# Optimization experiments

Measured on AMD Instinct MI355X. Metric: run time of the kernel, lower is better.

The kernel has to match this reference:

```python
import jax, jax.numpy as jnp
import numpy as np

B, C, D, H, W = 2, 128, 16, 16, 16

def setup_inputs() -> dict:
    key = jax.random.key(0)
    ks = jax.random.split(key, 7)
    s = 0.02
    return {
        "x": jax.random.normal(ks[0], (B, C, D, H, W), jnp.float32),
        "Wq": jax.random.normal(ks[1], (C, C), jnp.float32) * s,
        "bq": jax.random.normal(ks[2], (C,), jnp.float32) * s,
        "Wk": jax.random.normal(ks[3], (C, C), jnp.float32) * s,
        "bk": jax.random.normal(ks[4], (C,), jnp.float32) * s,
        "Wv": jax.random.normal(ks[5], (C, C), jnp.float32) * s,
        "bv": jax.random.normal(ks[6], (C,), jnp.float32) * s,
    }

def reference(x, Wq, bq, Wk, bk, Wv, bv):
    b, c, d, h, w = x.shape
    n = d * h * w
    xf = x.reshape(b, c, n)  # [B, C, N]
    # 1x1x1 Conv3d == per-voxel linear over channels
    q = jnp.einsum('oc,bcn->bon', Wq, xf) + bq[None, :, None]
    k = jnp.einsum('oc,bcn->bon', Wk, xf) + bk[None, :, None]
    v = jnp.einsum('oc,bcn->bon', Wv, xf) + bv[None, :, None]
    # energy[b,n,m] = sum_c q[b,c,n] * k[b,c,m]  (no scale, as in source)
    energy = jnp.einsum('bcn,bcm->bnm', q, k)
    attention = jax.nn.softmax(energy, axis=-1)
    # out[b,c,n] = sum_m v[b,c,m] * attention[b,n,m]
    out = jnp.einsum('bcm,bnm->bcn', v, attention)
    return out.reshape(b, c, d, h, w)
```

## Files before the change

### kernel.cpp

```cpp
#include <hip/hip_runtime.h>


typedef __bf16 bf16x8 __attribute__((ext_vector_type(8)));
typedef __bf16 bf16x4v __attribute__((ext_vector_type(4)));
typedef float  f32x4  __attribute__((ext_vector_type(4)));

#define LDP 136
#define LDO 33
#define QB_STRIDE 132
#define VB_STRIDE 36

constexpr int CB = 128;
constexpr int NB = 4096;
constexpr int BB = 2;

__device__ __forceinline__ bf16x8 ldfrag(const __bf16* lds, int row, int koff, int ld) {
  return *(const bf16x8*)(lds + row * ld + koff);
}

__device__ __forceinline__ unsigned cvt_pk_bf16(float lo, float hi) {
  unsigned w;
  asm("v_cvt_pk_bf16_f32 %0, %1, %2" : "=v"(w) : "v"(lo), "v"(hi));
  return w;
}

__global__ __launch_bounds__(256) void qkv_fused_kernel(
    const float* __restrict__ x,
    const float* __restrict__ Wq, const float* __restrict__ bq,
    const float* __restrict__ Wk, const float* __restrict__ bk,
    const float* __restrict__ Wv, const float* __restrict__ bv,
    __bf16* __restrict__ Qt, __bf16* __restrict__ Kt, __bf16* __restrict__ Vo)
{
  extern __shared__ __align__(16) char smem_raw[];
  __bf16* xT = (__bf16*)smem_raw;
  __bf16* Wl = xT + 32 * LDP;
  float* bounce = (float*)(Wl + 128 * LDP);

  const int b  = blockIdx.y;
  const int n0 = blockIdx.x * 32;
  const int t  = threadIdx.x;
  const int lane = t & 63, w = t >> 6;
  const int l15 = lane & 15, quad = lane >> 4;
  const int nstrip = (w & 1) * 16;
  const int obase  = (w >> 1) * 64;

#pragma unroll
  for (int u = 0; u < 4; u++) {
    int v = t + u * 256;
    int c = v >> 3, i4 = v & 7;
    float4 d = *(const float4*)(x + (size_t)(b * CB + c) * NB + n0 + i4 * 4);
    xT[(i4 * 4 + 0) * LDP + c] = (__bf16)d.x;
    xT[(i4 * 4 + 1) * LDP + c] = (__bf16)d.y;
    xT[(i4 * 4 + 2) * LDP + c] = (__bf16)d.z;
    xT[(i4 * 4 + 3) * LDP + c] = (__bf16)d.w;
  }

  auto store_m = [&](int mm) {
    if (mm < 2) {
      const float* bp = (mm == 0) ? bq : bk;
      const float qs = (mm == 0) ? 1.4426950408889634f : 1.0f;
      __bf16* O = (mm == 0) ? Qt : Kt;
#pragma unroll
      for (int u = 0; u < 2; u++) {
        int v = t + u * 256;
        int n = v >> 4, c8 = (v & 15) * 8;
        f32x4 p0 = *(const f32x4*)(bounce + n * QB_STRIDE + c8);
        f32x4 p1 = *(const f32x4*)(bounce + n * QB_STRIDE + c8 + 4);
        float4 b0 = *(const float4*)(bp + c8);
        float4 b1 = *(const float4*)(bp + c8 + 4);
        bf16x8 o8;
        o8[0] = (__bf16)((p0[0] + b0.x) * qs);
        o8[1] = (__bf16)((p0[1] + b0.y) * qs);
        o8[2] = (__bf16)((p0[2] + b0.z) * qs);
        o8[3] = (__bf16)((p0[3] + b0.w) * qs);
        o8[4] = (__bf16)((p1[0] + b1.x) * qs);
        o8[5] = (__bf16)((p1[1] + b1.y) * qs);
        o8[6] = (__bf16)((p1[2] + b1.z) * qs);
        o8[7] = (__bf16)((p1[3] + b1.w) * qs);
        *(bf16x8*)(O + (size_t)(b * NB + n0 + n) * CB + c8) = o8;
      }
    } else {
#pragma unroll
      for (int u = 0; u < 2; u++) {
        int v = t + u * 256;
        int o = v >> 2, n8 = (v & 3) * 8;
        float bias = bv[o];
        f32x4 p0 = *(const f32x4*)(bounce + o * VB_STRIDE + n8);
        f32x4 p1 = *(const f32x4*)(bounce + o * VB_STRIDE + n8 + 4);
        bf16x8 o8;
        o8[0] = (__bf16)(p0[0] + bias);
        o8[1] = (__bf16)(p0[1] + bias);
        o8[2] = (__bf16)(p0[2] + bias);
        o8[3] = (__bf16)(p0[3] + bias);
        o8[4] = (__bf16)(p1[0] + bias);
        o8[5] = (__bf16)(p1[1] + bias);
        o8[6] = (__bf16)(p1[2] + bias);
        o8[7] = (__bf16)(p1[3] + bias);
        *(bf16x8*)(Vo + (size_t)(b * CB + o) * NB + n0 + n8) = o8;
      }
    }
  };

#pragma unroll
  for (int m = 0; m < 3; m++) {
    const float* W = (m == 0) ? Wq : (m == 1) ? Wk : Wv;
#pragma unroll
    for (int u = 0; u < 16; u++) {
      int v = t + u * 256;
      int o = v >> 5, c4 = v & 31;
      float4 d = *(const float4*)(W + o * 128 + c4 * 4);
      bf16x4v uu = {(__bf16)d.x, (__bf16)d.y, (__bf16)d.z, (__bf16)d.w};
      *(bf16x4v*)(Wl + o * LDP + c4 * 4) = uu;
    }
    if (m > 0) store_m(m - 1);
    __syncthreads();

    if (m < 2) {
      f32x4 acc[4] = {(f32x4)0.0f, (f32x4)0.0f, (f32x4)0.0f, (f32x4)0.0f};
#pragma unroll
      for (int ks = 0; ks < 4; ks++) {
        int koff = ks * 32 + quad * 8;
        bf16x8 a = ldfrag(xT, nstrip + l15, koff, LDP);
#pragma unroll
        for (int ct = 0; ct < 4; ct++) {
          bf16x8 bb = ldfrag(Wl, obase + ct * 16 + l15, koff, LDP);
          acc[ct] = __builtin_amdgcn_mfma_f32_16x16x32_bf16(a, bb, acc[ct], 0, 0, 0);
        }
      }
#pragma unroll
      for (int ct = 0; ct < 4; ct++)
#pragma unroll
        for (int r = 0; r < 4; r++)
          bounce[(nstrip + quad * 4 + r) * QB_STRIDE + obase + ct * 16 + l15] =
              acc[ct][r];
    } else {
      f32x4 acc[4] = {(f32x4)0.0f, (f32x4)0.0f, (f32x4)0.0f, (f32x4)0.0f};
#pragma unroll
      for (int ks = 0; ks < 4; ks++) {
        int koff = ks * 32 + quad * 8;
        bf16x8 bb = ldfrag(xT, nstrip + l15, koff, LDP);
#pragma unroll
        for (int rr = 0; rr < 4; rr++) {
          bf16x8 a = ldfrag(Wl, obase + rr * 16 + l15, koff, LDP);
          acc[rr] = __builtin_amdgcn_mfma_f32_16x16x32_bf16(a, bb, acc[rr], 0, 0, 0);
        }
      }
#pragma unroll
      for (int rr = 0; rr < 4; rr++)
#pragma unroll
        for (int r = 0; r < 4; r++)
          bounce[(obase + rr * 16 + quad * 4 + r) * VB_STRIDE + nstrip + l15] =
              acc[rr][r];
    }
    __syncthreads();
  }
  store_m(2);
}

__global__ __launch_bounds__(256, 2) void attn_part_kernel(
    const __bf16* __restrict__ Qt,
    const __bf16* __restrict__ Kt,
    const __bf16* __restrict__ Vo,
    __bf16* __restrict__ Opart, float* __restrict__ Ll, int ksz)
{
  extern __shared__ __align__(16) char smem_raw[];

  const int b  = blockIdx.y;
  const int q0 = blockIdx.x * 128;
  const int s  = blockIdx.z;
  const int k_base = s * ksz;
  const int nit = ksz >> 6;
  const int t  = threadIdx.x;
  const int lane = t & 63, w = t >> 6;
  const int l15 = lane & 15, quad = lane >> 4;
  const int row0 = w * 32;
  const int xsw = (l15 & 7) << 4;

  bf16x8 qf[2][4];
#pragma unroll
  for (int qt = 0; qt < 2; qt++)
#pragma unroll
    for (int cb = 0; cb < 4; cb++)
      qf[qt][cb] = *(const bf16x8*)(Qt +
          (size_t)(b * NB + q0 + row0 + qt * 16 + l15) * CB + cb * 32 + quad * 8);

  bf16x8 kr[4], vr[4];
  auto load_tile = [&](int m0) {
#pragma unroll
    for (int u = 0; u < 4; u++) {
      int v = t + u * 256;
      int j = v >> 4, c8 = v & 15;
      kr[u] = *(const bf16x8*)(Kt + (size_t)(b * NB + m0 + j) * CB + c8 * 8);
    }
#pragma unroll
    for (int u = 0; u < 4; u++) {
      int v = t + u * 256;
      int c = v >> 3, j8 = v & 7;
      vr[u] = *(const bf16x8*)(Vo + (size_t)(b * CB + c) * NB + m0 + j8 * 8);
    }
  };
  auto write_tile = [&](int bf) {
    char* Kn = smem_raw + bf * 32768;
    char* Vn = Kn + 16384;
#pragma unroll
    for (int u = 0; u < 4; u++) {
      int v = t + u * 256;
      int j = v >> 4, c8 = v & 15;
      *(bf16x8*)(Kn + j * 256 + ((c8 * 16) ^ ((j & 7) << 4))) = kr[u];
    }
#pragma unroll
    for (int u = 0; u < 4; u++) {
      int v = t + u * 256;
      int c = v >> 3, j8 = v & 7;
      *(bf16x8*)(Vn + c * 128 + ((j8 * 16) ^ ((c & 7) << 4))) = vr[u];
    }
  };

  float lsum[2] = {0.0f, 0.0f};
  f32x4 o_acc[2][8];
#pragma unroll
  for (int qt = 0; qt < 2; qt++)
#pragma unroll
    for (int tt = 0; tt < 8; tt++) o_acc[qt][tt] = (f32x4)0.0f;

  load_tile(k_base);
  write_tile(0);
  __syncthreads();

  int cur = 0;
  for (int it = 0; it < nit; it++) {
    if (it + 1 < nit) load_tile(k_base + (it + 1) * 64);

    const char* Kc = smem_raw + cur * 32768;
    const char* Vc = Kc + 16384;

    f32x4 sacc[2][4];
#pragma unroll
    for (int qt = 0; qt < 2; qt++)
#pragma unroll
      for (int kt = 0; kt < 4; kt++) sacc[qt][kt] = (f32x4)0.0f;
#pragma unroll
    for (int cb = 0; cb < 4; cb++) {
      const int xo = (cb * 64 + quad * 16) ^ xsw;
#pragma unroll
      for (int kt = 0; kt < 4; kt++) {
        bf16x8 af = *(const bf16x8*)(Kc + (kt * 16 + l15) * 256 + xo);
        sacc[0][kt] = __builtin_amdgcn_mfma_f32_16x16x32_bf16(af, qf[0][cb], sacc[0][kt], 0, 0, 0);
        sacc[1][kt] = __builtin_amdgcn_mfma_f32_16x16x32_bf16(af, qf[1][cb], sacc[1][kt], 0, 0, 0);
      }
    }

    bf16x8 pa[2][2];
#pragma unroll
    for (int qt = 0; qt < 2; qt++) {
      unsigned d[4][2];
#pragma unroll
      for (int kt = 0; kt < 4; kt++) {
        float p0 = exp2f(sacc[qt][kt][0]);
        float p1 = exp2f(sacc[qt][kt][1]);
        float p2 = exp2f(sacc[qt][kt][2]);
        float p3 = exp2f(sacc[qt][kt][3]);
        lsum[qt] += (p0 + p1) + (p2 + p3);
        d[kt][0] = cvt_pk_bf16(p0, p1);
        d[kt][1] = cvt_pk_bf16(p2, p3);
      }
#pragma unroll
      for (int ks = 0; ks < 2; ks++) {
        unsigned a0 = d[2 * ks][0], a1 = d[2 * ks][1];
        unsigned b0 = d[2 * ks + 1][0], b1 = d[2 * ks + 1][1];
        asm("v_permlane32_swap_b32 %0, %1" : "+v"(a0), "+v"(b0));
        asm("v_permlane16_swap_b32 %0, %1" : "+v"(a0), "+v"(b0));
        asm("v_permlane32_swap_b32 %0, %1" : "+v"(a1), "+v"(b1));
        asm("v_permlane16_swap_b32 %0, %1" : "+v"(a1), "+v"(b1));
        union { unsigned u[4]; bf16x8 v; } pk;
        pk.u[0] = a0; pk.u[1] = a1; pk.u[2] = b0; pk.u[3] = b1;
        pa[qt][ks] = pk.v;
      }
    }

#pragma unroll
    for (int ks = 0; ks < 2; ks++) {
      const int xo = (ks * 64 + quad * 16) ^ xsw;
#pragma unroll
      for (int tt = 0; tt < 8; tt++) {
        bf16x8 bb = *(const bf16x8*)(Vc + (tt * 16 + l15) * 128 + xo);
        o_acc[0][tt] = __builtin_amdgcn_mfma_f32_16x16x32_bf16(pa[0][ks], bb, o_acc[0][tt], 0, 0, 0);
        o_acc[1][tt] = __builtin_amdgcn_mfma_f32_16x16x32_bf16(pa[1][ks], bb, o_acc[1][tt], 0, 0, 0);
      }
    }

    if (it + 1 < nit) {
      write_tile(cur ^ 1);
      __syncthreads();
      cur ^= 1;
    }
  }

#pragma unroll
  for (int qt = 0; qt < 2; qt++) {
    lsum[qt] += __shfl_xor(lsum[qt], 16);
    lsum[qt] += __shfl_xor(lsum[qt], 32);
  }

  const size_t obase = ((size_t)(s * BB + b) * NB + q0) * CB;
#pragma unroll
  for (int qt = 0; qt < 2; qt++)
#pragma unroll
    for (int tt = 0; tt < 8; tt++)
#pragma unroll
      for (int r = 0; r < 4; r++)
        Opart[obase + (size_t)(row0 + qt * 16 + quad * 4 + r) * CB + tt * 16 + l15] =
            (__bf16)o_acc[qt][tt][r];
  if (quad == 0) {
    const size_t lbase = (size_t)(s * BB + b) * NB + q0 + row0;
#pragma unroll
    for (int qt = 0; qt < 2; qt++)
      Ll[lbase + qt * 16 + l15] = lsum[qt];
  }
}

__global__ __launch_bounds__(256) void combine_kernel(
    const __bf16* __restrict__ Opart, const float* __restrict__ Ll,
    float* __restrict__ out, int nsplit)
{
  extern __shared__ __align__(16) char smem_raw[];
  float* Olf = (float*)smem_raw;

  const int b  = blockIdx.y;
  const int n0 = blockIdx.x * 64;
  const int c0 = blockIdx.z * 32;
  const int t  = threadIdx.x;
  const int i  = t >> 2;
  const int cc = (t & 3) * 8;

  float L = 0.0f;
  for (int s = 0; s < nsplit; s++)
    L += Ll[(size_t)(s * BB + b) * NB + n0 + i];

  float acc[8];
#pragma unroll
  for (int u = 0; u < 8; u++) acc[u] = 0.0f;
  for (int s = 0; s < nsplit; s++) {
    bf16x8 d = *(const bf16x8*)(Opart +
        ((size_t)(s * BB + b) * NB + n0 + i) * CB + c0 + cc);
#pragma unroll
    for (int u = 0; u < 8; u++) acc[u] += (float)d[u];
  }
  float invL = 1.0f / L;
#pragma unroll
  for (int u = 0; u < 8; u++) Olf[i * LDO + cc + u] = acc[u] * invL;
  __syncthreads();

  for (int v = t; v < 512; v += 256) {
    int c = v >> 4, i4 = v & 15;
    float4 d;
    d.x = Olf[(i4 * 4 + 0) * LDO + c];
    d.y = Olf[(i4 * 4 + 1) * LDO + c];
    d.z = Olf[(i4 * 4 + 2) * LDO + c];
    d.w = Olf[(i4 * 4 + 3) * LDO + c];
    *(float4*)(out + (size_t)(b * CB + c0 + c) * NB + n0 + i4 * 4) = d;
  }
}

extern "C" void kernel_launch(void* const* d_in, const int* in_sizes, int n_in,
                              void* d_out, int out_size, void* d_ws, size_t ws_size,
                              hipStream_t stream) {
  const float* x  = (const float*)d_in[0];
  const float* Wq = (const float*)d_in[1];
  const float* bq = (const float*)d_in[2];
  const float* Wk = (const float*)d_in[3];
  const float* bk = (const float*)d_in[4];
  const float* Wv = (const float*)d_in[5];
  const float* bv = (const float*)d_in[6];
  float* out = (float*)d_out;

  const size_t qkv_elems = (size_t)BB * NB * CB;
  __bf16* Qt = (__bf16*)d_ws;
  __bf16* Kt = Qt + qkv_elems;
  __bf16* Vo = Kt + qkv_elems;
  char* ws_tail = (char*)(Vo + qkv_elems);
  size_t tail_sz = ws_size - 3 * qkv_elems * sizeof(__bf16);

  const size_t per_split = (size_t)BB * NB * CB * 2 + (size_t)BB * NB * 4;
  int nsplit = 8;
  while (nsplit > 1 && (size_t)nsplit * per_split > tail_sz) nsplit >>= 1;

  __bf16* Opart = (__bf16*)ws_tail;
  float*  Ll = (float*)(Opart + (size_t)nsplit * BB * NB * CB);
  const int ksz = NB / nsplit;

  const int qkv_smem  = 32 * LDP * 2 + 128 * LDP * 2 + 128 * VB_STRIDE * 4;
  const int attn_smem = 65536;
  const int comb_smem = 64 * LDO * 4;

  qkv_fused_kernel<<<dim3(NB / 32, BB), 256, qkv_smem, stream>>>(
      x, Wq, bq, Wk, bk, Wv, bv, Qt, Kt, Vo);
  attn_part_kernel<<<dim3(NB / 128, BB, nsplit), 256, attn_smem, stream>>>(
      Qt, Kt, Vo, Opart, Ll, ksz);
  combine_kernel<<<dim3(NB / 64, BB, 4), 256, comb_smem, stream>>>(
      Opart, Ll, out, nsplit);
}
```

Measured before the change: 109.6 us.

## Use 512-thread attention blocks with fixed 256-key splits and two-phase staging

The attention kernel now runs 8 waves per block covering 256 queries, with the key range fixed at 256 per split (16 splits). K/V are staged in two 128-key phases into one buffer guarded by barriers, replacing the register-prefetched double buffer. The aim is more reuse of each staged K/V tile across more query rows and more parallelism from the extra splits. In exchange, global loads no longer overlap compute, partial-output traffic grows with the larger split count, and the workspace-size check is removed, so a small workspace is no longer guarded against.

Result: slower. 120.9 us (+10.4%).

```diff
diff --git a/kernel.cpp b/kernel.cpp
--- a/kernel.cpp
+++ b/kernel.cpp
@@ -13,6 +13,8 @@
 constexpr int CB = 128;
 constexpr int NB = 4096;
 constexpr int BB = 2;
+constexpr int KSZ = 256;
+constexpr int NSPLIT = NB / KSZ;
 
 __device__ __forceinline__ bf16x8 ldfrag(const __bf16* lds, int row, int koff, int ld) {
   return *(const bf16x8*)(lds + row * ld + koff);
@@ -157,19 +159,20 @@
   store_m(2);
 }
 
-__global__ __launch_bounds__(256, 2) void attn_part_kernel(
+__global__ __launch_bounds__(512, 2) void attn_part_kernel(
     const __bf16* __restrict__ Qt,
     const __bf16* __restrict__ Kt,
     const __bf16* __restrict__ Vo,
-    __bf16* __restrict__ Opart, float* __restrict__ Ll, int ksz)
+    __bf16* __restrict__ Opart, float* __restrict__ Ll)
 {
   extern __shared__ __align__(16) char smem_raw[];
+  char* Kl = smem_raw;
+  char* Vl = smem_raw + 32768;
 
   const int b  = blockIdx.y;
-  const int q0 = blockIdx.x * 128;
+  const int q0 = blockIdx.x * 256;
   const int s  = blockIdx.z;
-  const int k_base = s * ksz;
-  const int nit = ksz >> 6;
+  const int k_base = s * KSZ;
   const int t  = threadIdx.x;
   const int lane = t & 63, w = t >> 6;
   const int l15 = lane & 15, quad = lane >> 4;
@@ -184,35 +187,21 @@
       qf[qt][cb] = *(const bf16x8*)(Qt +
           (size_t)(b * NB + q0 + row0 + qt * 16 + l15) * CB + cb * 32 + quad * 8);
 
-  bf16x8 kr[4], vr[4];
-  auto load_tile = [&](int m0) {
+  auto stage_phase = [&](int p) {
+    const int m0 = k_base + p * 128;
 #pragma unroll
     for (int u = 0; u < 4; u++) {
-      int v = t + u * 256;
+      int v = t + u * 512;
       int j = v >> 4, c8 = v & 15;
-      kr[u] = *(const bf16x8*)(Kt + (size_t)(b * NB + m0 + j) * CB + c8 * 8);
+      bf16x8 d = *(const bf16x8*)(Kt + (size_t)(b * NB + m0 + j) * CB + c8 * 8);
+      *(bf16x8*)(Kl + j * 256 + ((c8 * 16) ^ ((j & 7) << 4))) = d;
     }
 #pragma unroll
     for (int u = 0; u < 4; u++) {
-      int v = t + u * 256;
-      int c = v >> 3, j8 = v & 7;
-      vr[u] = *(const bf16x8*)(Vo + (size_t)(b * CB + c) * NB + m0 + j8 * 8);
-    }
-  };
-  auto write_tile = [&](int bf) {
-    char* Kn = smem_raw + bf * 32768;
-    char* Vn = Kn + 16384;
-#pragma unroll
-    for (int u = 0; u < 4; u++) {
-      int v = t + u * 256;
-      int j = v >> 4, c8 = v & 15;
-      *(bf16x8*)(Kn + j * 256 + ((c8 * 16) ^ ((j & 7) << 4))) = kr[u];
-    }
-#pragma unroll
-    for (int u = 0; u < 4; u++) {
-      int v = t + u * 256;
-      int c = v >> 3, j8 = v & 7;
-      *(bf16x8*)(Vn + c * 128 + ((j8 * 16) ^ ((c & 7) << 4))) = vr[u];
+      int v = t + u * 512;
+      int c = v >> 4, k8 = v & 15;
+      bf16x8 d = *(const bf16x8*)(Vo + (size_t)(b * CB + c) * NB + m0 + k8 * 8);
+      *(bf16x8*)(Vl + c * 256 + ((k8 * 16) ^ ((c & 7) << 4))) = d;
     }
   };
 
@@ -223,76 +212,75 @@
 #pragma unroll
     for (int tt = 0; tt < 8; tt++) o_acc[qt][tt] = (f32x4)0.0f;
 
-  load_tile(k_base);
-  write_tile(0);
+  stage_phase(0);
   __syncthreads();
 
-  int cur = 0;
-  for (int it = 0; it < nit; it++) {
-    if (it + 1 < nit) load_tile(k_base + (it + 1) * 64);
-
-    const char* Kc = smem_raw + cur * 32768;
-    const char* Vc = Kc + 16384;
-
-    f32x4 sacc[2][4];
-#pragma unroll
-    for (int qt = 0; qt < 2; qt++)
-#pragma unroll
-      for (int kt = 0; kt < 4; kt++) sacc[qt][kt] = (f32x4)0.0f;
-#pragma unroll
-    for (int cb = 0; cb < 4; cb++) {
-      const int xo = (cb * 64 + quad * 16) ^ xsw;
-#pragma unroll
-      for (int kt = 0; kt < 4; kt++) {
-        bf16x8 af = *(const bf16x8*)(Kc + (kt * 16 + l15) * 256 + xo);
-        sacc[0][kt] = __builtin_amdgcn_mfma_f32_16x16x32_bf16(af, qf[0][cb], sacc[0][kt], 0, 0, 0);
-        sacc[1][kt] = __builtin_amdgcn_mfma_f32_16x16x32_bf16(af, qf[1][cb], sacc[1][kt], 0, 0, 0);
-      }
-    }
-
-    bf16x8 pa[2][2];
-#pragma unroll
-    for (int qt = 0; qt < 2; qt++) {
-      unsigned d[4][2];
-#pragma unroll
-      for (int kt = 0; kt < 4; kt++) {
-        float p0 = exp2f(sacc[qt][kt][0]);
-        float p1 = exp2f(sacc[qt][kt][1]);
-        float p2 = exp2f(sacc[qt][kt][2]);
-        float p3 = exp2f(sacc[qt][kt][3]);
-        lsum[qt] += (p0 + p1) + (p2 + p3);
-        d[kt][0] = cvt_pk_bf16(p0, p1);
-        d[kt][1] = cvt_pk_bf16(p2, p3);
-      }
+#pragma unroll
+  for (int p = 0; p < 2; p++) {
+    if (p == 1) {
+      __syncthreads();
+      stage_phase(1);
+      __syncthreads();
+    }
+
+#pragma unroll
+    for (int ch = 0; ch < 2; ch++) {
+      const char* Kc = Kl + ch * 64 * 256;
+
+      f32x4 sacc[2][4];
+#pragma unroll
+      for (int qt = 0; qt < 2; qt++)
+#pragma unroll
+        for (int kt = 0; kt < 4; kt++) sacc[qt][kt] = (f32x4)0.0f;
+#pragma unroll
+      for (int cb = 0; cb < 4; cb++) {
+        const int xo = (cb * 64 + quad * 16) ^ xsw;
+#pragma unroll
+        for (int kt = 0; kt < 4; kt++) {
+          bf16x8 af = *(const bf16x8*)(Kc + (kt * 16 + l15) * 256 + xo);
+          sacc[0][kt] = __builtin_amdgcn_mfma_f32_16x16x32_bf16(af, qf[0][cb], sacc[0][kt], 0, 0, 0);
+          sacc[1][kt] = __builtin_amdgcn_mfma_f32_16x16x32_bf16(af, qf[1][cb], sacc[1][kt], 0, 0, 0);
+        }
+      }
+
+      bf16x8 pa[2][2];
+#pragma unroll
+      for (int qt = 0; qt < 2; qt++) {
+        unsigned d[4][2];
+#pragma unroll
+        for (int kt = 0; kt < 4; kt++) {
+          float p0 = exp2f(sacc[qt][kt][0]);
+          float p1 = exp2f(sacc[qt][kt][1]);
+          float p2 = exp2f(sacc[qt][kt][2]);
+          float p3 = exp2f(sacc[qt][kt][3]);
+          lsum[qt] += (p0 + p1) + (p2 + p3);
+          d[kt][0] = cvt_pk_bf16(p0, p1);
+          d[kt][1] = cvt_pk_bf16(p2, p3);
+        }
+#pragma unroll
+        for (int ks = 0; ks < 2; ks++) {
+          unsigned a0 = d[2 * ks][0], a1 = d[2 * ks][1];
+          unsigned b0 = d[2 * ks + 1][0], b1 = d[2 * ks + 1][1];
+          asm("v_permlane32_swap_b32 %0, %1" : "+v"(a0), "+v"(b0));
+          asm("v_permlane16_swap_b32 %0, %1" : "+v"(a0), "+v"(b0));
+          asm("v_permlane32_swap_b32 %0, %1" : "+v"(a1), "+v"(b1));
+          asm("v_permlane16_swap_b32 %0, %1" : "+v"(a1), "+v"(b1));
+          union { unsigned u[4]; bf16x8 v; } pk;
+          pk.u[0] = a0; pk.u[1] = a1; pk.u[2] = b0; pk.u[3] = b1;
+          pa[qt][ks] = pk.v;
+        }
+      }
+
 #pragma unroll
       for (int ks = 0; ks < 2; ks++) {
-        unsigned a0 = d[2 * ks][0], a1 = d[2 * ks][1];
-        unsigned b0 = d[2 * ks + 1][0], b1 = d[2 * ks + 1][1];
-        asm("v_permlane32_swap_b32 %0, %1" : "+v"(a0), "+v"(b0));
-        asm("v_permlane16_swap_b32 %0, %1" : "+v"(a0), "+v"(b0));
-        asm("v_permlane32_swap_b32 %0, %1" : "+v"(a1), "+v"(b1));
-        asm("v_permlane16_swap_b32 %0, %1" : "+v"(a1), "+v"(b1));
-        union { unsigned u[4]; bf16x8 v; } pk;
-        pk.u[0] = a0; pk.u[1] = a1; pk.u[2] = b0; pk.u[3] = b1;
-        pa[qt][ks] = pk.v;
-      }
-    }
-
-#pragma unroll
-    for (int ks = 0; ks < 2; ks++) {
-      const int xo = (ks * 64 + quad * 16) ^ xsw;
-#pragma unroll
-      for (int tt = 0; tt < 8; tt++) {
-        bf16x8 bb = *(const bf16x8*)(Vc + (tt * 16 + l15) * 128 + xo);
-        o_acc[0][tt] = __builtin_amdgcn_mfma_f32_16x16x32_bf16(pa[0][ks], bb, o_acc[0][tt], 0, 0, 0);
-        o_acc[1][tt] = __builtin_amdgcn_mfma_f32_16x16x32_bf16(pa[1][ks], bb, o_acc[1][tt], 0, 0, 0);
-      }
-    }
-
-    if (it + 1 < nit) {
-      write_tile(cur ^ 1);
-      __syncthreads();
-      cur ^= 1;
+        const int xo = ((ch * 8 + ks * 4 + quad) * 16) ^ xsw;
+#pragma unroll
+        for (int tt = 0; tt < 8; tt++) {
+          bf16x8 bb = *(const bf16x8*)(Vl + (tt * 16 + l15) * 256 + xo);
+          o_acc[0][tt] = __builtin_amdgcn_mfma_f32_16x16x32_bf16(pa[0][ks], bb, o_acc[0][tt], 0, 0, 0);
+          o_acc[1][tt] = __builtin_amdgcn_mfma_f32_16x16x32_bf16(pa[1][ks], bb, o_acc[1][tt], 0, 0, 0);
+        }
+      }
     }
   }
 
@@ -379,15 +367,9 @@
   __bf16* Kt = Qt + qkv_elems;
   __bf16* Vo = Kt + qkv_elems;
   char* ws_tail = (char*)(Vo + qkv_elems);
-  size_t tail_sz = ws_size - 3 * qkv_elems * sizeof(__bf16);
-
-  const size_t per_split = (size_t)BB * NB * CB * 2 + (size_t)BB * NB * 4;
-  int nsplit = 8;
-  while (nsplit > 1 && (size_t)nsplit * per_split > tail_sz) nsplit >>= 1;
 
   __bf16* Opart = (__bf16*)ws_tail;
-  float*  Ll = (float*)(Opart + (size_t)nsplit * BB * NB * CB);
-  const int ksz = NB / nsplit;
+  float*  Ll = (float*)(Opart + (size_t)NSPLIT * BB * NB * CB);
 
   const int qkv_smem  = 32 * LDP * 2 + 128 * LDP * 2 + 128 * VB_STRIDE * 4;
   const int attn_smem = 65536;
@@ -395,8 +377,8 @@
 
   qkv_fused_kernel<<<dim3(NB / 32, BB), 256, qkv_smem, stream>>>(
       x, Wq, bq, Wk, bk, Wv, bv, Qt, Kt, Vo);
-  attn_part_kernel<<<dim3(NB / 128, BB, nsplit), 256, attn_smem, stream>>>(
-      Qt, Kt, Vo, Opart, Ll, ksz);
+  attn_part_kernel<<<dim3(NB / 256, BB, NSPLIT), 512, attn_smem, stream>>>(
+      Qt, Kt, Vo, Opart, Ll);
   combine_kernel<<<dim3(NB / 64, BB, 4), 256, comb_smem, stream>>>(
-      Opart, Ll, out, nsplit);
-}
+      Opart, Ll, out, NSPLIT);
+}
```
